# Kernel tuning notes

Measured on AMD Instinct MI355X. Metric: run time of the kernel, lower is better.

## Reference

```python
import jax, jax.numpy as jnp
import numpy as np

S, B, I, H = 256, 512, 46, 256  # seqlen, batch, i_dim, h_dim
EPS = 1e-5


def setup_inputs() -> dict:
    key = jax.random.key(0)
    ks = iter(jax.random.split(key, 64))
    nrm = lambda shape, s=0.05: jax.random.normal(next(ks), shape, dtype=jnp.float32) * s
    inp = {}
    inp['X'] = jax.random.normal(next(ks), (S, B, I), dtype=jnp.float32)
    inp['M'] = (jax.random.uniform(next(ks), (S, B, I)) > 0.5).astype(jnp.float32)
    inp['mask'] = (jax.random.uniform(next(ks), (S, B)) > 0.1).astype(jnp.float32)
    C = I - 6  # 40 clinical channels
    inp['i2h_w'] = nrm((H, 6)); inp['i2h_b'] = nrm((H,))
    inp['comb_w'] = nrm((C, 2 * C)); inp['comb_b'] = nrm((C,))
    inp['down_w'] = nrm((H, C)); inp['down_b'] = nrm((H,))
    inp['conv1_w'] = nrm((H, C)); inp['conv1_b'] = nrm((H,))
    inp['conv2_w'] = nrm((H, H)); inp['conv2_b'] = nrm((H,))
    inp['bn1_g'] = jnp.ones((H,), jnp.float32); inp['bn1_b'] = jnp.zeros((H,), jnp.float32)
    inp['bn2_g'] = jnp.ones((H,), jnp.float32); inp['bn2_b'] = jnp.zeros((H,), jnp.float32)
    for p in ('r1', 'r2'):
        inp[p + '_wih'] = nrm((3 * H, H)); inp[p + '_whh'] = nrm((3 * H, H))
        inp[p + '_bih'] = nrm((3 * H,)); inp[p + '_bhh'] = nrm((3 * H,))
        inp[p + '_cw'] = nrm((H, 2 * H)); inp[p + '_cb'] = nrm((H,))
    inp['ln1_g'] = jnp.ones((H,), jnp.float32); inp['ln1_b'] = jnp.zeros((H,), jnp.float32)
    inp['ln2_g'] = jnp.ones((H,), jnp.float32); inp['ln2_b'] = jnp.zeros((H,), jnp.float32)
    inp['ln3_g'] = jnp.ones((8,), jnp.float32); inp['ln3_b'] = jnp.zeros((8,), jnp.float32)
    inp['nn1_w'] = nrm((8, H)); inp['nn1_b'] = nrm((8,))
    inp['nn2_w'] = nrm((2, 8)); inp['nn2_b'] = nrm((2,))
    return inp


def _bn(x, g, b):
    # BatchNorm1d in training mode: stats over (seq, batch) per channel, biased var
    mu = x.mean((0, 1))
    var = x.var((0, 1))
    return (x - mu) * jax.lax.rsqrt(var + EPS) * g + b


def _ln(x, g, b):
    mu = x.mean(-1, keepdims=True)
    var = x.var(-1, keepdims=True)
    return (x - mu) * jax.lax.rsqrt(var + EPS) * g + b


def _modgru(Xs, h0, mask, wih, whh, bih, bhh, cw, cb):
    # precompute input-gate projections for all timesteps: [S,B,3H]
    gi = jnp.einsum('sbi,gi->sbg', Xs, wih) + bih

    def step(h, inp):
        x, g, m = inp  # x:[B,H], g:[B,3H], m:[B]
        gh = h @ whh.T + bhh
        ir, iz, inn = jnp.split(g, 3, axis=-1)
        hr, hz, hn = jnp.split(gh, 3, axis=-1)
        r = jax.nn.sigmoid(ir + hr)
        z = jax.nn.sigmoid(iz + hz)
        n = jnp.tanh(inn + r * hn)
        h_new = (1.0 - z) * n + z * h  # GRUCell update
        mm = m[:, None]
        h = h_new * mm + h * (1.0 - mm)  # mask blend
        out = jnp.concatenate([x, h], axis=-1) @ cw.T + cb  # com2
        return h, out

    _, outs = jax.lax.scan(step, h0, (Xs, gi, mask))
    return outs


def reference(X, M, mask, i2h_w, i2h_b, comb_w, comb_b, down_w, down_b,
              conv1_w, conv1_b, conv2_w, conv2_b, bn1_g, bn1_b, bn2_g, bn2_b,
              r1_wih, r1_whh, r1_bih, r1_bhh, r1_cw, r1_cb,
              r2_wih, r2_whh, r2_bih, r2_bhh, r2_cw, r2_cb,
              ln1_g, ln1_b, ln2_g, ln2_b, ln3_g, ln3_b,
              nn1_w, nn1_b, nn2_w, nn2_b):
    p_info = X[0, :, -6:]          # [B,6] static patient info
    Xin = X[:, :, :-6]             # [S,B,40]
    Min = M[:, :, :-6]
    h0 = p_info @ i2h_w.T + i2h_b  # [B,H]
    res = Xin @ down_w.T + down_b  # [S,B,H]
    Xc = jnp.concatenate([Xin, Min], axis=-1) @ comb_w.T + comb_b
    # kernel-size-1 convs == per-timestep linear (layout kept [S,B,C])
    out = Xc @ conv1_w.T + conv1_b
    out = jax.nn.relu(_bn(out, bn1_g, bn1_b))
    out = out @ conv2_w.T + conv2_b
    out = _bn(out, bn2_g, bn2_b)
    hx = out + res
    hx = _ln(_modgru(hx, h0, mask, r1_wih, r1_whh, r1_bih, r1_bhh, r1_cw, r1_cb), ln1_g, ln1_b)
    hx = _ln(_modgru(hx, h0, mask, r2_wih, r2_whh, r2_bih, r2_bhh, r2_cw, r2_cb), ln2_g, ln2_b)
    hx = jax.nn.relu(hx @ nn1_w.T + nn1_b)
    hx = _ln(hx, ln3_g, ln3_b)
    return hx @ nn2_w.T + nn2_b  # [S,B,2]
```

## Files before the change

### kernel.cpp

```cpp
#include <hip/hip_runtime.h>
#include <hip/hip_bf16.h>

#define SS 256
#define BB 512
#define II 46
#define HH 256
#define CC 40
#define SB (SS*BB)
#define G3 (3*HH)
#define EPSF 1e-5f

typedef __attribute__((ext_vector_type(8))) short bf16x8;
typedef __attribute__((ext_vector_type(4))) float f32x4;

__device__ __forceinline__ unsigned short f2bf_rne(float f){
  unsigned u = __float_as_uint(f);
  unsigned r = (u + 0x7FFFu + ((u >> 16) & 1u)) >> 16;
  return (unsigned short)r;
}
__device__ __forceinline__ float bf2f(unsigned short b){
  return __uint_as_float(((unsigned)b) << 16);
}
__device__ __forceinline__ void cvt8(const float* v, bf16x8& hi, bf16x8& lo){
  #pragma unroll
  for (int e=0;e<8;e++){
    unsigned short hb = f2bf_rne(v[e]);
    hi[e] = (short)hb;
    lo[e] = (short)f2bf_rne(v[e] - bf2f(hb));
  }
}

__global__ void pack_xm_chunk_k(const float* __restrict__ X, const float* __restrict__ Mi,
                                float* __restrict__ XM, long long r0, int Rr){
  long long idx = (long long)blockIdx.x*blockDim.x + threadIdx.x;
  if (idx >= (long long)Rr*80) return;
  int r = (int)(idx / 80);
  int c = (int)(idx - (long long)r*80);
  long long gr = r0 + r;
  float v;
  if (c < CC) v = X[gr*II + c];
  else        v = Mi[gr*II + (c - CC)];
  XM[idx] = v;
}

__global__ void h0_k(const float* __restrict__ X, const float* __restrict__ w,
                     const float* __restrict__ bias, float* __restrict__ h1c,
                     float* __restrict__ h2c){
  int b = blockIdx.x, jj = threadIdx.x;
  const float* p = X + (long long)b*II + (II - 6);
  float acc = bias[jj];
  #pragma unroll
  for (int c2=0;c2<6;c2++) acc = fmaf(p[c2], w[jj*6 + c2], acc);
  h1c[(long long)b*HH + jj] = acc;
  h2c[(long long)b*HH + jj] = acc;
}

__global__ void whht_k(const float* __restrict__ w, float* __restrict__ wt){
  int idx = blockIdx.x*blockDim.x + threadIdx.x;
  if (idx >= G3*HH) return;
  int u = idx / HH, k = idx - u*HH;
  wt[(size_t)k*G3 + u] = w[idx];
}

template<int MODE>
__global__ void gemm_tn(const float* __restrict__ A, int lda,
                        const float* __restrict__ W, int ldw,
                        const float* __restrict__ bias,
                        float* __restrict__ Co, int ldc,
                        int Mrows, int N, int K)
{
  __shared__ __align__(16) float As[32][132];
  __shared__ __align__(16) float Ws[32][132];
  const int m0 = blockIdx.x*128, n0 = blockIdx.y*128;
  const int t  = threadIdx.x;
  const int tm = t >> 4, tn = t & 15;
  float acc[8][8];
  #pragma unroll
  for (int i=0;i<8;i++)
    #pragma unroll
    for (int j2=0;j2<8;j2++) acc[i][j2] = 0.f;

  for (int k0=0;k0<K;k0+=32){
    #pragma unroll
    for (int u=0;u<16;u++){
      int idx = u*256 + t;
      int r = idx >> 5, c = idx & 31;
      int gk = k0 + c;
      float av = 0.f, wv = 0.f;
      if (gk < K){
        int gm = m0 + r;
        if (gm < Mrows) av = A[(long long)gm*lda + gk];
        int gn = n0 + r;
        if (gn < N)     wv = W[(long long)gn*ldw + gk];
      }
      As[c][r] = av;
      Ws[c][r] = wv;
    }
    __syncthreads();
    #pragma unroll
    for (int kk=0;kk<32;kk++){
      const float4 a0 = *(const float4*)&As[kk][tm*8];
      const float4 a1 = *(const float4*)&As[kk][tm*8+4];
      const float4 b0 = *(const float4*)&Ws[kk][tn*8];
      const float4 b1 = *(const float4*)&Ws[kk][tn*8+4];
      const float av[8] = {a0.x,a0.y,a0.z,a0.w,a1.x,a1.y,a1.z,a1.w};
      const float bv[8] = {b0.x,b0.y,b0.z,b0.w,b1.x,b1.y,b1.z,b1.w};
      #pragma unroll
      for (int i=0;i<8;i++)
        #pragma unroll
        for (int j2=0;j2<8;j2++) acc[i][j2] = fmaf(av[i], bv[j2], acc[i][j2]);
    }
    __syncthreads();
  }
  #pragma unroll
  for (int i=0;i<8;i++){
    int gm = m0 + tm*8 + i;
    if (gm < Mrows){
      #pragma unroll
      for (int j2=0;j2<8;j2++){
        int gn = n0 + tn*8 + j2;
        if (gn < N){
          long long oi = (long long)gm*ldc + gn;
          float val = acc[i][j2] + bias[gn];
          if (MODE == 1) val = fmaxf(val, 0.f);
          if (MODE == 2) val += Co[oi];
          Co[oi] = val;
        }
      }
    }
  }
}

template<int MODE>
__global__ __launch_bounds__(256) void gemm_mf(
    const float* __restrict__ A, int lda,
    const float* __restrict__ W, int ldw,
    const float* __restrict__ bias,
    float* __restrict__ Co, int ldc,
    int N, int K)
{
  __shared__ __align__(16) unsigned short Ah[128*32];
  __shared__ __align__(16) unsigned short Al[128*32];
  __shared__ __align__(16) unsigned short Bh[128*32];
  __shared__ __align__(16) unsigned short Bl[128*32];
  const int t = threadIdx.x;
  const int m0 = blockIdx.x*128, n0 = blockIdx.y*128;
  const int lane = t & 63, w = t >> 6;
  const int wm = (w & 1)*64, wn = (w >> 1)*64;
  const int fr = lane & 15, fg = lane >> 4;

  f32x4 acc[4][4];
  #pragma unroll
  for (int i=0;i<4;i++)
    #pragma unroll
    for (int j=0;j<4;j++){ f32x4 z; z[0]=0;z[1]=0;z[2]=0;z[3]=0; acc[i][j]=z; }

  for (int k0=0; k0<K; k0+=32){
    #pragma unroll
    for (int cc=0; cc<2; cc++){
      const int c   = t + cc*256;
      const int row = c >> 2, kg = c & 3;
      const int byte = row*64 + ((kg*16) ^ (((row>>1)&3)<<4));
      {
        const float* ap = A + (size_t)(m0+row)*lda + k0 + kg*8;
        float v[8];
        *(float4*)&v[0] = *(const float4*)ap;
        *(float4*)&v[4] = *(const float4*)(ap+4);
        bf16x8 hi, lo; cvt8(v, hi, lo);
        *(bf16x8*)((char*)Ah + byte) = hi;
        *(bf16x8*)((char*)Al + byte) = lo;
      }
      {
        const float* bp = W + (size_t)(n0+row)*ldw + k0 + kg*8;
        float v[8];
        *(float4*)&v[0] = *(const float4*)bp;
        *(float4*)&v[4] = *(const float4*)(bp+4);
        bf16x8 hi, lo; cvt8(v, hi, lo);
        *(bf16x8*)((char*)Bh + byte) = hi;
        *(bf16x8*)((char*)Bl + byte) = lo;
      }
    }
    __syncthreads();
    bf16x8 ahi[4], alo[4], bhi[4], blo[4];
    #pragma unroll
    for (int mt=0; mt<4; mt++){
      const int r = wm + mt*16 + fr;
      const int byte = r*64 + ((fg*16) ^ (((r>>1)&3)<<4));
      ahi[mt] = *(const bf16x8*)((const char*)Ah + byte);
      alo[mt] = *(const bf16x8*)((const char*)Al + byte);
    }
    #pragma unroll
    for (int nt=0; nt<4; nt++){
      const int r = wn + nt*16 + fr;
      const int byte = r*64 + ((fg*16) ^ (((r>>1)&3)<<4));
      bhi[nt] = *(const bf16x8*)((const char*)Bh + byte);
      blo[nt] = *(const bf16x8*)((const char*)Bl + byte);
    }
    #pragma unroll
    for (int mt=0; mt<4; mt++)
      #pragma unroll
      for (int nt=0; nt<4; nt++){
        acc[mt][nt] = __builtin_amdgcn_mfma_f32_16x16x32_bf16(alo[mt], bhi[nt], acc[mt][nt], 0,0,0);
        acc[mt][nt] = __builtin_amdgcn_mfma_f32_16x16x32_bf16(ahi[mt], blo[nt], acc[mt][nt], 0,0,0);
        acc[mt][nt] = __builtin_amdgcn_mfma_f32_16x16x32_bf16(ahi[mt], bhi[nt], acc[mt][nt], 0,0,0);
      }
    __syncthreads();
  }

  #pragma unroll
  for (int mt=0; mt<4; mt++){
    #pragma unroll
    for (int nt=0; nt<4; nt++){
      const int col = n0 + wn + nt*16 + fr;
      const float bv = bias[col];
      #pragma unroll
      for (int i=0;i<4;i++){
        const int row = m0 + wm + mt*16 + fg*4 + i;
        const size_t oi = (size_t)row*ldc + col;
        float val = acc[mt][nt][i] + bv;
        if (MODE == 2) val += Co[oi];
        Co[oi] = val;
      }
    }
  }
}

__global__ __launch_bounds__(256) void gemm_mf_dual(
    const float* __restrict__ A1, const float* __restrict__ A2,
    const float* __restrict__ W,
    const float* __restrict__ bias,
    float* __restrict__ Co, int ldc, int N)
{
  __shared__ __align__(16) unsigned short Ah[128*32];
  __shared__ __align__(16) unsigned short Al[128*32];
  __shared__ __align__(16) unsigned short Bh[128*32];
  __shared__ __align__(16) unsigned short Bl[128*32];
  const int t = threadIdx.x;
  const int m0 = blockIdx.x*128, n0 = blockIdx.y*128;
  const int lane = t & 63, w = t >> 6;
  const int wm = (w & 1)*64, wn = (w >> 1)*64;
  const int fr = lane & 15, fg = lane >> 4;

  f32x4 acc[4][4];
  #pragma unroll
  for (int i=0;i<4;i++)
    #pragma unroll
    for (int j=0;j<4;j++){ f32x4 z; z[0]=0;z[1]=0;z[2]=0;z[3]=0; acc[i][j]=z; }

  for (int k0=0; k0<2*HH; k0+=32){
    const float* Abase = (k0 < HH) ? A1 : A2;
    const int    kofs  = (k0 < HH) ? k0 : (k0 - HH);
    #pragma unroll
    for (int cc=0; cc<2; cc++){
      const int c   = t + cc*256;
      const int row = c >> 2, kg = c & 3;
      const int byte = row*64 + ((kg*16) ^ (((row>>1)&3)<<4));
      {
        const float* ap = Abase + (size_t)(m0+row)*HH + kofs + kg*8;
        float v[8];
        *(float4*)&v[0] = *(const float4*)ap;
        *(float4*)&v[4] = *(const float4*)(ap+4);
        bf16x8 hi, lo; cvt8(v, hi, lo);
        *(bf16x8*)((char*)Ah + byte) = hi;
        *(bf16x8*)((char*)Al + byte) = lo;
      }
      {
        const float* bp = W + (size_t)(n0+row)*(2*HH) + k0 + kg*8;
        float v[8];
        *(float4*)&v[0] = *(const float4*)bp;
        *(float4*)&v[4] = *(const float4*)(bp+4);
        bf16x8 hi, lo; cvt8(v, hi, lo);
        *(bf16x8*)((char*)Bh + byte) = hi;
        *(bf16x8*)((char*)Bl + byte) = lo;
      }
    }
    __syncthreads();
    bf16x8 ahi[4], alo[4], bhi[4], blo[4];
    #pragma unroll
    for (int mt=0; mt<4; mt++){
      const int r = wm + mt*16 + fr;
      const int byte = r*64 + ((fg*16) ^ (((r>>1)&3)<<4));
      ahi[mt] = *(const bf16x8*)((const char*)Ah + byte);
      alo[mt] = *(const bf16x8*)((const char*)Al + byte);
    }
    #pragma unroll
    for (int nt=0; nt<4; nt++){
      const int r = wn + nt*16 + fr;
      const int byte = r*64 + ((fg*16) ^ (((r>>1)&3)<<4));
      bhi[nt] = *(const bf16x8*)((const char*)Bh + byte);
      blo[nt] = *(const bf16x8*)((const char*)Bl + byte);
    }
    #pragma unroll
    for (int mt=0; mt<4; mt++)
      #pragma unroll
      for (int nt=0; nt<4; nt++){
        acc[mt][nt] = __builtin_amdgcn_mfma_f32_16x16x32_bf16(alo[mt], bhi[nt], acc[mt][nt], 0,0,0);
        acc[mt][nt] = __builtin_amdgcn_mfma_f32_16x16x32_bf16(ahi[mt], blo[nt], acc[mt][nt], 0,0,0);
        acc[mt][nt] = __builtin_amdgcn_mfma_f32_16x16x32_bf16(ahi[mt], bhi[nt], acc[mt][nt], 0,0,0);
      }
    __syncthreads();
  }

  #pragma unroll
  for (int mt=0; mt<4; mt++){
    #pragma unroll
    for (int nt=0; nt<4; nt++){
      const int col = n0 + wn + nt*16 + fr;
      const float bv = bias[col];
      #pragma unroll
      for (int i=0;i<4;i++){
        const int row = m0 + wm + mt*16 + fg*4 + i;
        const size_t oi = (size_t)row*ldc + col;
        Co[oi] = acc[mt][nt][i] + bv;
      }
    }
  }
}

__global__ void bn_partial_k(const float* __restrict__ Xc, float* __restrict__ ps,
                             float* __restrict__ pq, int pblk0){
  int blk = blockIdx.x, t = threadIdx.x;
  long long base = (long long)blk*512*HH;
  float s = 0.f, q = 0.f;
  for (int r=0;r<512;r++){
    float v = Xc[base + (long long)r*HH + t];
    s += v; q = fmaf(v, v, q);
  }
  ps[(pblk0+blk)*HH + t] = s;
  pq[(pblk0+blk)*HH + t] = q;
}

__global__ void bn_final_k(const float* __restrict__ ps, const float* __restrict__ pq,
                           const float* __restrict__ g, const float* __restrict__ b,
                           float* __restrict__ sc, float* __restrict__ sh){
  int t = threadIdx.x;
  double s = 0.0, q = 0.0;
  for (int i=0;i<256;i++){ s += (double)ps[i*HH + t]; q += (double)pq[i*HH + t]; }
  double mu  = s / (double)SB;
  double var = q / (double)SB - mu*mu;
  float scv = (float)((double)g[t] / sqrt(var + 1e-5));
  sc[t] = scv;
  sh[t] = (float)((double)b[t] - mu*(double)scv);
}

__global__ void fold_k(const float* __restrict__ w, const float* __restrict__ b,
                       const float* __restrict__ sc, const float* __restrict__ sh,
                       float* __restrict__ wf, float* __restrict__ bf, int K){
  int idx = blockIdx.x*blockDim.x + threadIdx.x;
  if (idx < 256*K){ int o = idx / K; wf[idx] = w[idx]*sc[o]; }
  if (idx < 256)  bf[idx] = b[idx]*sc[idx] + sh[idx];
}

__global__ void ln_rows_k(const float* __restrict__ Xi, float* __restrict__ Xo,
                          const float* __restrict__ g, const float* __restrict__ b){
  long long row = blockIdx.x;
  int t = threadIdx.x;
  float v = Xi[row*HH + t];
  float s = v, q = v*v;
  #pragma unroll
  for (int o=32;o>0;o>>=1){ s += __shfl_down(s,o); q += __shfl_down(q,o); }
  __shared__ float ssm[4], qqm[4];
  int w = t >> 6;
  if ((t & 63) == 0){ ssm[w] = s; qqm[w] = q; }
  __syncthreads();
  if (t == 0){ ssm[0] = ssm[0]+ssm[1]+ssm[2]+ssm[3]; qqm[0] = qqm[0]+qqm[1]+qqm[2]+qqm[3]; }
  __syncthreads();
  s = ssm[0]; q = qqm[0];
  float mu  = s * (1.f/HH);
  float var = q * (1.f/HH) - mu*mu;
  float rs  = rsqrtf(var + EPSF);
  Xo[row*HH + t] = (v - mu)*rs*g[t] + b[t];
}

#define DOT4(hv,A0,A1,A2,A3) \
  A0=fmaf(hv.x,w0.x,A0); A0=fmaf(hv.y,w1.x,A0); A0=fmaf(hv.z,w2.x,A0); A0=fmaf(hv.w,w3.x,A0); \
  A1=fmaf(hv.x,w0.y,A1); A1=fmaf(hv.y,w1.y,A1); A1=fmaf(hv.z,w2.y,A1); A1=fmaf(hv.w,w3.y,A1); \
  A2=fmaf(hv.x,w0.z,A2); A2=fmaf(hv.y,w1.z,A2); A2=fmaf(hv.z,w2.z,A2); A2=fmaf(hv.w,w3.z,A2); \
  A3=fmaf(hv.x,w0.w,A3); A3=fmaf(hv.y,w1.w,A3); A3=fmaf(hv.z,w2.w,A3); A3=fmaf(hv.w,w3.w,A3);

__global__ __launch_bounds__(768) void gru_scan_ks_k(
  const float* __restrict__ gi,
  const float* __restrict__ whhT,
  const float* __restrict__ bhh,
  const float* __restrict__ mask0,
  float* __restrict__ hcar,
  float* __restrict__ Hh,
  int nst)
{
  const int t  = threadIdx.x;
  const int b0 = blockIdx.x*4;
  const int cg = t % 192;
  const int ks = t / 192;
  const int c0 = cg*4;
  const int k0 = ks*64;
  __shared__ __align__(16) float h[4][260];
  __shared__ __align__(16) float part[4][4][776];
  __shared__ float mkz[4];

  const int uj = t & 255;
  const int ur = t >> 8;
  if (t < 512){
    h[ur  ][uj] = hcar[(size_t)(b0+ur  )*HH + uj];
    h[ur+2][uj] = hcar[(size_t)(b0+ur+2)*HH + uj];
  }
  float br=0.f, bz=0.f, bn_=0.f;
  if (t < 512){ br = bhh[uj]; bz = bhh[uj+HH]; bn_ = bhh[uj+2*HH]; }
  __syncthreads();

  const float* wbase = whhT + (size_t)k0*G3 + c0;

  for (int st=0; st<nst; ++st){
    float i0r=0,i0z=0,i0n=0, i1r=0,i1z=0,i1n=0;
    if (t < 512){
      const size_t ga = ((size_t)st*BB + b0 + ur  )*G3 + uj;
      const size_t gb = ((size_t)st*BB + b0 + ur+2)*G3 + uj;
      i0r=gi[ga]; i0z=gi[ga+HH]; i0n=gi[ga+2*HH];
      i1r=gi[gb]; i1z=gi[gb+HH]; i1n=gi[gb+2*HH];
    }
    if (t < 4) mkz[t] = mask0[(size_t)st*BB + b0 + t];

    float a00=0,a01=0,a02=0,a03=0;
    float a10=0,a11=0,a12=0,a13=0;
    float a20=0,a21=0,a22=0,a23=0;
    float a30=0,a31=0,a32=0,a33=0;
    #pragma unroll 4
    for (int kk=0; kk<64; kk+=4){
      const float4 w0 = *(const float4*)(wbase + (size_t)(kk  )*G3);
      const float4 w1 = *(const float4*)(wbase + (size_t)(kk+1)*G3);
      const float4 w2 = *(const float4*)(wbase + (size_t)(kk+2)*G3);
      const float4 w3 = *(const float4*)(wbase + (size_t)(kk+3)*G3);
      const float4 h0 = *(const float4*)&h[0][k0+kk];
      const float4 h1 = *(const float4*)&h[1][k0+kk];
      const float4 h2 = *(const float4*)&h[2][k0+kk];
      const float4 h3 = *(const float4*)&h[3][k0+kk];
      DOT4(h0,a00,a01,a02,a03);
      DOT4(h1,a10,a11,a12,a13);
      DOT4(h2,a20,a21,a22,a23);
      DOT4(h3,a30,a31,a32,a33);
    }
    *(float4*)&part[ks][0][c0] = make_float4(a00,a01,a02,a03);
    *(float4*)&part[ks][1][c0] = make_float4(a10,a11,a12,a13);
    *(float4*)&part[ks][2][c0] = make_float4(a20,a21,a22,a23);
    *(float4*)&part[ks][3][c0] = make_float4(a30,a31,a32,a33);
    __syncthreads();

    if (t < 512){
      {
        const int r_ = ur;
        const float ar = part[0][r_][uj]+part[1][r_][uj]+part[2][r_][uj]+part[3][r_][uj] + br;
        const float az = part[0][r_][uj+HH]+part[1][r_][uj+HH]+part[2][r_][uj+HH]+part[3][r_][uj+HH] + bz;
        const float an = part[0][r_][uj+2*HH]+part[1][r_][uj+2*HH]+part[2][r_][uj+2*HH]+part[3][r_][uj+2*HH] + bn_;
        const float rr = 1.f/(1.f + __expf(-(i0r + ar)));
        const float zz = 1.f/(1.f + __expf(-(i0z + az)));
        const float nn = tanhf(fmaf(rr, an, i0n));
        const float hold = h[r_][uj];
        const float m = mkz[r_];
        const float hnew = (1.f - zz)*nn + zz*hold;
        const float hv = hnew*m + hold*(1.f - m);
        h[r_][uj] = hv;
        Hh[((size_t)st*BB + b0 + r_)*HH + uj] = hv;
      }
      {
        const int r_ = ur + 2;
        const float ar = part[0][r_][uj]+part[1][r_][uj]+part[2][r_][uj]+part[3][r_][uj] + br;
        const float az = part[0][r_][uj+HH]+part[1][r_][uj+HH]+part[2][r_][uj+HH]+part[3][r_][uj+HH] + bz;
        const float an = part[0][r_][uj+2*HH]+part[1][r_][uj+2*HH]+part[2][r_][uj+2*HH]+part[3][r_][uj+2*HH] + bn_;
        const float rr = 1.f/(1.f + __expf(-(i1r + ar)));
        const float zz = 1.f/(1.f + __expf(-(i1z + az)));
        const float nn = tanhf(fmaf(rr, an, i1n));
        const float hold = h[r_][uj];
        const float m = mkz[r_];
        const float hnew = (1.f - zz)*nn + zz*hold;
        const float hv = hnew*m + hold*(1.f - m);
        h[r_][uj] = hv;
        Hh[((size_t)st*BB + b0 + r_)*HH + uj] = hv;
      }
    }
    __syncthreads();
  }
  if (t < 512){
    hcar[(size_t)(b0+ur  )*HH + uj] = h[ur  ][uj];
    hcar[(size_t)(b0+ur+2)*HH + uj] = h[ur+2][uj];
  }
}

__global__ void head_ln_k(const float* __restrict__ hx,
                          const float* __restrict__ g2, const float* __restrict__ b2,
                          const float* __restrict__ w1, const float* __restrict__ b1,
                          const float* __restrict__ g3, const float* __restrict__ b3,
                          const float* __restrict__ w2, const float* __restrict__ b2h,
                          float* __restrict__ outp, long long r0){
  long long row = blockIdx.x;
  int t = threadIdx.x;
  float v = hx[row*HH + t];
  float s = v, q = v*v;
  #pragma unroll
  for (int o=32;o>0;o>>=1){ s += __shfl_down(s,o); q += __shfl_down(q,o); }
  __shared__ float ssm[4], qqm[4];
  int w = t >> 6;
  if ((t & 63) == 0){ ssm[w] = s; qqm[w] = q; }
  __syncthreads();
  if (t == 0){ ssm[0] = ssm[0]+ssm[1]+ssm[2]+ssm[3]; qqm[0] = qqm[0]+qqm[1]+qqm[2]+qqm[3]; }
  __syncthreads();
  s = ssm[0]; q = qqm[0];
  float mu  = s * (1.f/HH);
  float var = q * (1.f/HH) - mu*mu;
  float rs  = rsqrtf(var + EPSF);
  __shared__ float xs[HH];
  xs[t] = (v - mu)*rs*g2[t] + b2[t];
  __syncthreads();
  int o = t >> 5, l = t & 31;
  const float* wv = w1 + o*HH;
  float acc = 0.f;
  for (int k=l;k<HH;k+=32) acc = fmaf(xs[k], wv[k], acc);
  #pragma unroll
  for (int d=16;d>0;d>>=1) acc += __shfl_down(acc, d, 32);
  __shared__ float a8[8];
  if (l == 0) a8[o] = fmaxf(acc + b1[o], 0.f);
  __syncthreads();
  if (t == 0){
    float ss = 0.f;
    #pragma unroll
    for (int i=0;i<8;i++) ss += a8[i];
    float m8 = ss*0.125f;
    float qq = 0.f;
    #pragma unroll
    for (int i=0;i<8;i++){ float d = a8[i]-m8; qq = fmaf(d,d,qq); }
    float r8 = rsqrtf(qq*0.125f + EPSF);
    float y0 = b2h[0], y1 = b2h[1];
    #pragma unroll
    for (int i=0;i<8;i++){
      float vv = (a8[i]-m8)*r8*g3[i] + b3[i];
      y0 = fmaf(vv, w2[i],   y0);
      y1 = fmaf(vv, w2[8+i], y1);
    }
    outp[(r0+row)*2+0] = y0; outp[(r0+row)*2+1] = y1;
  }
}

extern "C" void kernel_launch(void* const* d_in, const int* in_sizes, int n_in,
                              void* d_out, int out_size, void* d_ws, size_t ws_size,
                              hipStream_t stream) {
  const float* X      = (const float*)d_in[0];
  const float* Mi     = (const float*)d_in[1];
  const float* mask   = (const float*)d_in[2];
  const float* i2h_w  = (const float*)d_in[3];
  const float* i2h_b  = (const float*)d_in[4];
  const float* comb_w = (const float*)d_in[5];
  const float* comb_b = (const float*)d_in[6];
  const float* down_w = (const float*)d_in[7];
  const float* down_b = (const float*)d_in[8];
  const float* conv1_w= (const float*)d_in[9];
  const float* conv1_b= (const float*)d_in[10];
  const float* conv2_w= (const float*)d_in[11];
  const float* conv2_b= (const float*)d_in[12];
  const float* bn1_g  = (const float*)d_in[13];
  const float* bn1_b  = (const float*)d_in[14];
  const float* bn2_g  = (const float*)d_in[15];
  const float* bn2_b  = (const float*)d_in[16];
  const float* r1_wih = (const float*)d_in[17];
  const float* r1_whh = (const float*)d_in[18];
  const float* r1_bih = (const float*)d_in[19];
  const float* r1_bhh = (const float*)d_in[20];
  const float* r1_cw  = (const float*)d_in[21];
  const float* r1_cb  = (const float*)d_in[22];
  const float* r2_wih = (const float*)d_in[23];
  const float* r2_whh = (const float*)d_in[24];
  const float* r2_bih = (const float*)d_in[25];
  const float* r2_bhh = (const float*)d_in[26];
  const float* r2_cw  = (const float*)d_in[27];
  const float* r2_cb  = (const float*)d_in[28];
  const float* ln1_g  = (const float*)d_in[29];
  const float* ln1_b  = (const float*)d_in[30];
  const float* ln2_g  = (const float*)d_in[31];
  const float* ln2_b  = (const float*)d_in[32];
  const float* ln3_g  = (const float*)d_in[33];
  const float* ln3_b  = (const float*)d_in[34];
  const float* nn1_w  = (const float*)d_in[35];
  const float* nn1_b  = (const float*)d_in[36];
  const float* nn2_w  = (const float*)d_in[37];
  const float* nn2_b  = (const float*)d_in[38];
  float* outp = (float*)d_out;

  const size_t tail_floats = 2*(size_t)BB*HH + 2*(size_t)256*HH + 2*HH
                           + (size_t)256*40 + 256 + (size_t)HH*HH + 256
                           + 2*(size_t)G3*HH + (size_t)SB*CC;
  int cands[6] = {256,128,64,32,16,8};
  int sc_chunk = 0;
  for (int ci=0; ci<6; ci++){
    size_t R = (size_t)512*cands[ci];
    size_t need = (R*1536 + tail_floats)*sizeof(float);
    if (need <= ws_size){ sc_chunk = cands[ci]; break; }
  }
  if (!sc_chunk) return;

  const size_t R = (size_t)512*sc_chunk;
  const int Ri = (int)R;
  const int nchunks = SB / Ri;

  float* wsf = (float*)d_ws;
  float* A   = wsf;
  float* GIc = A + R*HH;
  float* Cxp = GIc + R*G3;
  float* Ee  = Cxp + R*HH;
  float* tl  = Ee + R*HH;
  float* H1C = tl;
  float* H2C = H1C + (size_t)BB*HH;
  float* PS  = H2C + (size_t)BB*HH;
  float* PQ  = PS  + (size_t)256*HH;
  float* SCv = PQ  + (size_t)256*HH;
  float* SHv = SCv + HH;
  float* W1F = SHv + HH;
  float* B1F = W1F + (size_t)256*40;
  float* W2F = B1F + HH;
  float* B2F = W2F + (size_t)HH*HH;
  float* W1T = B2F + HH;
  float* W2T = W1T + (size_t)HH*G3;
  float* XcF = W2T + (size_t)HH*G3;

  whht_k<<<(G3*HH + 255)/256, 256, 0, stream>>>(r1_whh, W1T);
  whht_k<<<(G3*HH + 255)/256, 256, 0, stream>>>(r2_whh, W2T);

  const int PACKG = (Ri*80 + 255)/256;
  const int MB = Ri/128;

  for (int c=0;c<nchunks;c++){
    long long r0 = (long long)c*R;
    pack_xm_chunk_k<<<PACKG, 256, 0, stream>>>(X, Mi, Ee, r0, Ri);
    gemm_tn<0><<<dim3(MB,1), 256, 0, stream>>>(Ee, 80, comb_w, 80, comb_b, XcF + r0*CC, CC, Ri, CC, 80);
    gemm_tn<0><<<dim3(MB,2), 256, 0, stream>>>(XcF + r0*CC, CC, conv1_w, CC, conv1_b, Ee, HH, Ri, HH, CC);
    bn_partial_k<<<Ri/512, 256, 0, stream>>>(Ee, PS, PQ, (int)(r0/512));
  }
  bn_final_k<<<1, 256, 0, stream>>>(PS, PQ, bn1_g, bn1_b, SCv, SHv);
  fold_k<<<(256*40 + 255)/256, 256, 0, stream>>>(conv1_w, conv1_b, SCv, SHv, W1F, B1F, 40);

  for (int c=0;c<nchunks;c++){
    long long r0 = (long long)c*R;
    gemm_tn<1><<<dim3(MB,2), 256, 0, stream>>>(XcF + r0*CC, CC, W1F, CC, B1F, Ee, HH, Ri, HH, CC);
    gemm_mf<0><<<dim3(MB,2), 256, 0, stream>>>(Ee, HH, conv2_w, HH, conv2_b, A, HH, HH, HH);
    bn_partial_k<<<Ri/512, 256, 0, stream>>>(A, PS, PQ, (int)(r0/512));
  }
  bn_final_k<<<1, 256, 0, stream>>>(PS, PQ, bn2_g, bn2_b, SCv, SHv);
  fold_k<<<(256*256 + 255)/256, 256, 0, stream>>>(conv2_w, conv2_b, SCv, SHv, W2F, B2F, 256);

  h0_k<<<BB, HH, 0, stream>>>(X, i2h_w, i2h_b, H1C, H2C);

  for (int c=0;c<nchunks;c++){
    long long r0 = (long long)c*R;
    gemm_tn<0><<<dim3(MB,2), 256, 0, stream>>>(X + r0*II, II, down_w, CC, down_b, A, HH, Ri, HH, CC);
    gemm_tn<1><<<dim3(MB,2), 256, 0, stream>>>(XcF + r0*CC, CC, W1F, CC, B1F, Ee, HH, Ri, HH, CC);
    gemm_mf<2><<<dim3(MB,2), 256, 0, stream>>>(Ee, HH, W2F, HH, B2F, A, HH, HH, HH);
    gemm_mf<0><<<dim3(MB,6), 256, 0, stream>>>(A, HH, r1_wih, HH, r1_bih, GIc, G3, G3, HH);
    gru_scan_ks_k<<<BB/4, 768, 0, stream>>>(GIc, W1T, r1_bhh, mask + r0, H1C, Ee, sc_chunk);
    gemm_mf_dual<<<dim3(MB,2), 256, 0, stream>>>(A, Ee, r1_cw, r1_cb, Cxp, HH, HH);
    ln_rows_k<<<Ri, 256, 0, stream>>>(Cxp, Ee, ln1_g, ln1_b);
    gemm_mf<0><<<dim3(MB,6), 256, 0, stream>>>(Ee, HH, r2_wih, HH, r2_bih, GIc, G3, G3, HH);
    gru_scan_ks_k<<<BB/4, 768, 0, stream>>>(GIc, W2T, r2_bhh, mask + r0, H2C, A, sc_chunk);
    gemm_mf_dual<<<dim3(MB,2), 256, 0, stream>>>(Ee, A, r2_cw, r2_cb, Cxp, HH, HH);
    head_ln_k<<<Ri, 256, 0, stream>>>(Cxp, ln2_g, ln2_b, nn1_w, nn1_b, ln3_g, ln3_b, nn2_w, nn2_b, outp, r0);
  }
}
```

Measured before the change: 6.621 ms.

## Software-pipeline two GRU layers across chunks in one fused scan launch

Merges the layer-1 and layer-2 GRU recurrences into one kernel launch. Even blocks scan layer 1 on the current chunk while odd blocks scan layer 2 on the previous chunk, with a drain step after the loop. This doubles the blocks in flight during the latency-bound sequential scan and removes one serial scan per chunk. In exchange it needs extra workspace buffers (a second gate buffer and layer-2 hidden and input buffers), which can force a smaller chunk size, and it adds a pipeline epilogue.

```diff
diff --git a/kernel.cpp b/kernel.cpp
--- a/kernel.cpp
+++ b/kernel.cpp
@@ -378,17 +378,27 @@
   A2=fmaf(hv.x,w0.z,A2); A2=fmaf(hv.y,w1.z,A2); A2=fmaf(hv.z,w2.z,A2); A2=fmaf(hv.w,w3.z,A2); \
   A3=fmaf(hv.x,w0.w,A3); A3=fmaf(hv.y,w1.w,A3); A3=fmaf(hv.z,w2.w,A3); A3=fmaf(hv.w,w3.w,A3);
 
-__global__ __launch_bounds__(768) void gru_scan_ks_k(
-  const float* __restrict__ gi,
-  const float* __restrict__ whhT,
-  const float* __restrict__ bhh,
-  const float* __restrict__ mask0,
-  float* __restrict__ hcar,
-  float* __restrict__ Hh,
-  int nst)
+__global__ __launch_bounds__(768) void gru_scan_fused_k(
+  const float* __restrict__ gi1, const float* __restrict__ w1T,
+  const float* __restrict__ b1v, const float* __restrict__ m1v,
+  float* __restrict__ hc1, float* __restrict__ Hh1o, int nst1,
+  const float* __restrict__ gi2, const float* __restrict__ w2T,
+  const float* __restrict__ b2v, const float* __restrict__ m2v,
+  float* __restrict__ hc2, float* __restrict__ Hh2o, int nst2)
 {
+  const int gsel = blockIdx.x & 1;
+  const int blk  = blockIdx.x >> 1;
+  const float* gi    = gsel ? gi2 : gi1;
+  const float* whhT  = gsel ? w2T : w1T;
+  const float* bhh   = gsel ? b2v : b1v;
+  const float* mask0 = gsel ? m2v : m1v;
+  float* hcar        = gsel ? hc2 : hc1;
+  float* Hh          = gsel ? Hh2o : Hh1o;
+  const int nst      = gsel ? nst2 : nst1;
+  if (nst <= 0) return;
+
   const int t  = threadIdx.x;
-  const int b0 = blockIdx.x*4;
+  const int b0 = blk*4;
   const int cg = t % 192;
   const int ks = t / 192;
   const int c0 = cg*4;
@@ -589,7 +599,7 @@
   int sc_chunk = 0;
   for (int ci=0; ci<6; ci++){
     size_t R = (size_t)512*cands[ci];
-    size_t need = (R*1536 + tail_floats)*sizeof(float);
+    size_t need = (R*2816 + tail_floats)*sizeof(float);
     if (need <= ws_size){ sc_chunk = cands[ci]; break; }
   }
   if (!sc_chunk) return;
@@ -600,10 +610,13 @@
 
   float* wsf = (float*)d_ws;
   float* A   = wsf;
-  float* GIc = A + R*HH;
-  float* Cxp = GIc + R*G3;
+  float* GI1 = A + R*HH;
+  float* GI2 = GI1 + R*G3;
+  float* Cxp = GI2 + R*G3;
   float* Ee  = Cxp + R*HH;
-  float* tl  = Ee + R*HH;
+  float* Hh2 = Ee + R*HH;
+  float* Hx1 = Hh2 + R*HH;
+  float* tl  = Hx1 + R*HH;
   float* H1C = tl;
   float* H2C = H1C + (size_t)BB*HH;
   float* PS  = H2C + (size_t)BB*HH;
@@ -647,16 +660,28 @@
 
   for (int c=0;c<nchunks;c++){
     long long r0 = (long long)c*R;
+    long long rp = r0 - (long long)R;
     gemm_tn<0><<<dim3(MB,2), 256, 0, stream>>>(X + r0*II, II, down_w, CC, down_b, A, HH, Ri, HH, CC);
     gemm_tn<1><<<dim3(MB,2), 256, 0, stream>>>(XcF + r0*CC, CC, W1F, CC, B1F, Ee, HH, Ri, HH, CC);
     gemm_mf<2><<<dim3(MB,2), 256, 0, stream>>>(Ee, HH, W2F, HH, B2F, A, HH, HH, HH);
-    gemm_mf<0><<<dim3(MB,6), 256, 0, stream>>>(A, HH, r1_wih, HH, r1_bih, GIc, G3, G3, HH);
-    gru_scan_ks_k<<<BB/4, 768, 0, stream>>>(GIc, W1T, r1_bhh, mask + r0, H1C, Ee, sc_chunk);
+    gemm_mf<0><<<dim3(MB,6), 256, 0, stream>>>(A, HH, r1_wih, HH, r1_bih, GI1, G3, G3, HH);
+    gru_scan_fused_k<<<2*(BB/4), 768, 0, stream>>>(
+        GI1, W1T, r1_bhh, mask + r0, H1C, Ee, sc_chunk,
+        GI2, W2T, r2_bhh, (c > 0) ? (mask + rp) : mask, H2C, Hh2, (c > 0) ? sc_chunk : 0);
+    if (c > 0){
+      gemm_mf_dual<<<dim3(MB,2), 256, 0, stream>>>(Hx1, Hh2, r2_cw, r2_cb, Cxp, HH, HH);
+      head_ln_k<<<Ri, 256, 0, stream>>>(Cxp, ln2_g, ln2_b, nn1_w, nn1_b, ln3_g, ln3_b, nn2_w, nn2_b, outp, rp);
+    }
     gemm_mf_dual<<<dim3(MB,2), 256, 0, stream>>>(A, Ee, r1_cw, r1_cb, Cxp, HH, HH);
-    ln_rows_k<<<Ri, 256, 0, stream>>>(Cxp, Ee, ln1_g, ln1_b);
-    gemm_mf<0><<<dim3(MB,6), 256, 0, stream>>>(Ee, HH, r2_wih, HH, r2_bih, GIc, G3, G3, HH);
-    gru_scan_ks_k<<<BB/4, 768, 0, stream>>>(GIc, W2T, r2_bhh, mask + r0, H2C, A, sc_chunk);
-    gemm_mf_dual<<<dim3(MB,2), 256, 0, stream>>>(Ee, A, r2_cw, r2_cb, Cxp, HH, HH);
-    head_ln_k<<<Ri, 256, 0, stream>>>(Cxp, ln2_g, ln2_b, nn1_w, nn1_b, ln3_g, ln3_b, nn2_w, nn2_b, outp, r0);
-  }
-}
+    ln_rows_k<<<Ri, 256, 0, stream>>>(Cxp, Hx1, ln1_g, ln1_b);
+    gemm_mf<0><<<dim3(MB,6), 256, 0, stream>>>(Hx1, HH, r2_wih, HH, r2_bih, GI2, G3, G3, HH);
+  }
+  {
+    long long rl = (long long)(nchunks-1)*R;
+    gru_scan_fused_k<<<2*(BB/4), 768, 0, stream>>>(
+        GI1, W1T, r1_bhh, mask, H1C, Ee, 0,
+        GI2, W2T, r2_bhh, mask + rl, H2C, Hh2, sc_chunk);
+    gemm_mf_dual<<<dim3(MB,2), 256, 0, stream>>>(Hx1, Hh2, r2_cw, r2_cb, Cxp, HH, HH);
+    head_ln_k<<<Ri, 256, 0, stream>>>(Cxp, ln2_g, ln2_b, nn1_w, nn1_b, ln3_g, ln3_b, nn2_w, nn2_b, outp, rl);
+  }
+}
```

Result: no change. 6.660 ms (+0.6%).
